# Kernel tuning notes

Measured on AMD Instinct MI355X. Metric: run time of the kernel, lower is better.

The kernel has to match this reference:

```python
import jax, jax.numpy as jnp
import numpy as np

N = 50000
F = 96
E = 800000
H = 2
DEPTH = 3
LEAKY_ALPHA = 0.2  # tf.nn.leaky_relu default


def setup_inputs() -> dict:
    key = jax.random.key(0)
    k1, k2, k3, k4, k5, k6 = jax.random.split(key, 6)
    node_f = jax.random.normal(k1, (N, F), dtype=jnp.float32)
    rows = jax.random.randint(k2, (E,), 0, N, dtype=jnp.int64)
    cols = jax.random.randint(k3, (E,), 0, N, dtype=jnp.int64)
    adj_idx = jnp.stack([rows, cols], axis=-1)[None]  # [1, E, 2]
    diag = jnp.arange(N, dtype=jnp.int64)
    adj_self_idx = jnp.stack([diag, diag], axis=-1)  # [N, 2] self loops
    adj_self_val = jax.random.uniform(k4, (N,), dtype=jnp.float32)
    attn_self_k = jax.random.normal(k5, (H, F), dtype=jnp.float32) * 0.05
    attn_neigh_k = jax.random.normal(k6, (H, F), dtype=jnp.float32) * 0.05
    return {"node_f": node_f, "adj_idx": adj_idx, "adj_self_idx": adj_self_idx,
            "adj_self_val": adj_self_val, "attn_self_k": attn_self_k,
            "attn_neigh_k": attn_neigh_k}


def _segment_softmax(scores, seg, n):
    # softmax over the nonzero entries of each row (tf.sparse_softmax semantics)
    m = jax.ops.segment_max(scores, seg, num_segments=n)
    ex = jnp.exp(scores - m[seg])
    denom = jax.ops.segment_sum(ex, seg, num_segments=n)
    return ex / denom[seg]


def reference(node_f, adj_idx, adj_self_idx, adj_self_val, attn_self_k, attn_neigh_k):
    rows = adj_idx[0, :, 0]
    cols = adj_idx[0, :, 1]
    s_rows = adj_self_idx[:, 0]
    s_cols = adj_self_idx[:, 1]
    # features = adj_self @ node_f (sparse matmul)
    features = jax.ops.segment_sum(adj_self_val[:, None] * node_f[s_cols],
                                   s_rows, num_segments=N)
    features = jax.nn.relu(features)
    outputs = [features]
    for _ in range(DEPTH):
        def head_fn(a_s, a_n, feats=features):
            e_self = feats @ a_s    # [N]
            e_neigh = feats @ a_n   # [N]
            scores = jax.nn.leaky_relu(e_self[rows] + e_neigh[cols], LEAKY_ALPHA)
            att = _segment_softmax(scores, rows, N)  # [E]
            return jax.ops.segment_sum(att[:, None] * feats[cols], rows,
                                       num_segments=N)  # [N, F]
        heads = jax.vmap(head_fn)(attn_self_k, attn_neigh_k)  # [H, N, F]
        features = jax.nn.relu(jnp.mean(heads, axis=0))
        outputs.append(features)
    return jnp.concatenate(outputs, axis=-1)  # [N, F*(DEPTH+1)]
```

## Files before the change

kernel.cpp:

```cpp
#include <hip/hip_runtime.h>
#include <math.h>

#define NN 50000
#define FF 96
#define EE 800000
#define OF 384
#define GB 3125
#define FBU 48
#define CAP 64
#define NB 196
#define BCAP 4608
#define CHUNK 4082
#define SHARD 12500

__device__ __forceinline__ float grp_sum(float v) {
    for (int m = 8; m >= 1; m >>= 1) v += __shfl_xor(v, m, 64);
    return v;
}
__device__ __forceinline__ float lrelu(float x) { return x > 0.f ? x : 0.2f * x; }
__device__ __forceinline__ float bf_lo(unsigned u) { return __uint_as_float(u << 16); }
__device__ __forceinline__ float bf_hi(unsigned u) { return __uint_as_float(u & 0xffff0000u); }
__device__ __forceinline__ unsigned pack_bf(float a, float b) {
    unsigned ua = __float_as_uint(a), ub = __float_as_uint(b);
    ua = ua + 0x7fffu + ((ua >> 16) & 1u);
    ub = ub + 0x7fffu + ((ub >> 16) & 1u);
    return (ua >> 16) | (ub & 0xffff0000u);
}

__device__ __forceinline__ float grp_dot8(const float* a,
                                          const float* __restrict__ kf, int lg) {
    float s = 0.f;
    if (lg < 12) {
        float4 w0 = ((const float4*)kf)[2 * lg];
        float4 w1 = ((const float4*)kf)[2 * lg + 1];
        s = a[0] * w0.x + a[1] * w0.y + a[2] * w0.z + a[3] * w0.w +
            a[4] * w1.x + a[5] * w1.y + a[6] * w1.z + a[7] * w1.w;
    }
    return grp_sum(s);
}

template<int BF>
__global__ __launch_bounds__(256) void l0_phase1(const float* __restrict__ node_f,
                                                 const int* __restrict__ sidx,
                                                 const float* __restrict__ sval,
                                                 float* __restrict__ out,
                                                 unsigned* __restrict__ fb,
                                                 const float* __restrict__ ks,
                                                 const float* __restrict__ kn,
                                                 float2* __restrict__ ass,
                                                 float2* __restrict__ ann,
                                                 const int2* __restrict__ idx2,
                                                 int* __restrict__ bfill,
                                                 unsigned* __restrict__ buckets) {
    __shared__ int cnt[NB], basearr[NB], ofs[NB];
    int tid = threadIdx.x;
    if (blockIdx.x < NB) {
        int p = blockIdx.x;
        int start = p * CHUNK, end = min(start + CHUNK, EE);
        if (tid < NB) { cnt[tid] = 0; ofs[tid] = 0; }
        __syncthreads();
        for (int e = start + tid; e < end; e += 256)
            atomicAdd(&cnt[idx2[e].x >> 8], 1);
        __syncthreads();
        if (tid < NB)
            basearr[tid] = cnt[tid] ? atomicAdd(&bfill[tid], cnt[tid]) : 0;
        __syncthreads();
        for (int e = start + tid; e < end; e += 256) {
            int2 q = idx2[e];
            int b = q.x >> 8;
            int slot = basearr[b] + atomicAdd(&ofs[b], 1);
            if (slot < BCAP)
                buckets[(size_t)b * BCAP + slot] =
                    ((unsigned)(q.x & 255) << 16) | (unsigned)q.y;
        }
        return;
    }
    int g = tid >> 4, lg = tid & 15;
    int n = (blockIdx.x - NB) * 16 + g;
    if (n >= NN) return;
    int sr = sidx[2 * n];
    int sc = sidx[2 * n + 1];
    float v = sval[n];
    float a[8] = {0.f, 0.f, 0.f, 0.f, 0.f, 0.f, 0.f, 0.f};
    if (lg < 12) {
        const float4* xr4 = (const float4*)(node_f + (size_t)sc * FF);
        float4 x0 = xr4[2 * lg], x1 = xr4[2 * lg + 1];
        a[0] = fmaxf(v * x0.x, 0.f); a[1] = fmaxf(v * x0.y, 0.f);
        a[2] = fmaxf(v * x0.z, 0.f); a[3] = fmaxf(v * x0.w, 0.f);
        a[4] = fmaxf(v * x1.x, 0.f); a[5] = fmaxf(v * x1.y, 0.f);
        a[6] = fmaxf(v * x1.z, 0.f); a[7] = fmaxf(v * x1.w, 0.f);
        float4* op4 = (float4*)(out + (size_t)sr * OF);
        op4[2 * lg]     = make_float4(a[0], a[1], a[2], a[3]);
        op4[2 * lg + 1] = make_float4(a[4], a[5], a[6], a[7]);
        if (BF) {
            uint4 p;
            p.x = pack_bf(a[0], a[1]); p.y = pack_bf(a[2], a[3]);
            p.z = pack_bf(a[4], a[5]); p.w = pack_bf(a[6], a[7]);
            ((uint4*)(fb + (size_t)sr * FBU))[lg] = p;
        }
    }
    float p0 = grp_dot8(a, ks, lg);
    float p1 = grp_dot8(a, ks + FF, lg);
    float p2 = grp_dot8(a, kn, lg);
    float p3 = grp_dot8(a, kn + FF, lg);
    if (lg == 0) {
        ass[sr] = make_float2(p0, p1);
        ann[sr] = make_float2(p2, p3);
    }
}

__global__ __launch_bounds__(256) void bucket2csr(const int* __restrict__ bfill,
                                                  const unsigned* __restrict__ buckets,
                                                  int* __restrict__ fill,
                                                  unsigned short* __restrict__ csr) {
    __shared__ unsigned short lcsr[64 * CAP];
    __shared__ int lcnt[64 * 4], loff[64 * 4];
    int tid = threadIdx.x, b = blockIdx.x >> 2, q = blockIdx.x & 3;
    lcnt[tid] = 0;
    __syncthreads();
    int cnt = min(bfill[b], BCAP);
    const unsigned* bp = buckets + (size_t)b * BCAP;
    for (int i = tid; i < cnt; i += 256) {
        unsigned u = bp[i];
        int lr = u >> 16;
        if ((lr >> 6) == q)
            atomicAdd(&lcnt[(lr & 63) * 4 + (int)((u & 0xffffu) / SHARD)], 1);
    }
    __syncthreads();
    if (tid < 64) {
        int c0 = lcnt[tid * 4], c1 = lcnt[tid * 4 + 1];
        int c2 = lcnt[tid * 4 + 2], c3 = lcnt[tid * 4 + 3];
        loff[tid * 4] = 0;
        loff[tid * 4 + 1] = c0;
        loff[tid * 4 + 2] = c0 + c1;
        loff[tid * 4 + 3] = c0 + c1 + c2;
        int r = b * 256 + q * 64 + tid;
        if (r < NN) fill[r] = min(c0 + c1 + c2 + c3, CAP);
        lcnt[tid * 4] = 0; lcnt[tid * 4 + 1] = 0;
        lcnt[tid * 4 + 2] = 0; lcnt[tid * 4 + 3] = 0;
    }
    __syncthreads();
    for (int i = tid; i < cnt; i += 256) {
        unsigned u = bp[i];
        int lr = u >> 16;
        if ((lr >> 6) != q) continue;
        int col = u & 0xffffu, cls = col / SHARD, lrl = lr & 63;
        int pos = loff[lrl * 4 + cls] + atomicAdd(&lcnt[lrl * 4 + cls], 1);
        if (pos < CAP) lcsr[lrl * CAP + pos] = (unsigned short)col;
    }
    __syncthreads();
    const uint4* src = (const uint4*)lcsr;
    uint4* dst = (uint4*)(csr + ((size_t)b * 256 + q * 64) * CAP);
    for (int i = tid; i < 64 * CAP / 8; i += 256) dst[i] = src[i];
}

template<int BF>
__device__ __forceinline__ void agg_chunk(float cj, int colj, int nj, int gbase,
                                          const float* __restrict__ feats,
                                          const unsigned* __restrict__ fb, int lg,
                                          float* a) {
#pragma unroll 8
    for (int k = 0; k < nj; ++k) {
        float cc = __shfl(cj, gbase + k, 64);
        int col  = __shfl(colj, gbase + k, 64);
        if (lg < 12) {
            if (BF) {
                uint4 q = ((const uint4*)(fb + (size_t)col * FBU))[lg];
                a[0] += cc * bf_lo(q.x); a[1] += cc * bf_hi(q.x);
                a[2] += cc * bf_lo(q.y); a[3] += cc * bf_hi(q.y);
                a[4] += cc * bf_lo(q.z); a[5] += cc * bf_hi(q.z);
                a[6] += cc * bf_lo(q.w); a[7] += cc * bf_hi(q.w);
            } else {
                const float4* vp = (const float4*)(feats + (size_t)col * OF);
                float4 v0 = vp[2 * lg], v1 = vp[2 * lg + 1];
                a[0] += cc * v0.x; a[1] += cc * v0.y;
                a[2] += cc * v0.z; a[3] += cc * v0.w;
                a[4] += cc * v1.x; a[5] += cc * v1.y;
                a[6] += cc * v1.z; a[7] += cc * v1.w;
            }
        }
    }
}

template<int BF>
__global__ __launch_bounds__(256) void gat_layer(float* __restrict__ out, int l,
                                                 const int* __restrict__ fill,
                                                 const unsigned short* __restrict__ csr,
                                                 const float2* __restrict__ ass,
                                                 const float2* __restrict__ ann,
                                                 const unsigned* __restrict__ fb_in,
                                                 unsigned* __restrict__ fb_out,
                                                 const float* __restrict__ ks,
                                                 const float* __restrict__ kn,
                                                 float2* __restrict__ ass_out,
                                                 float2* __restrict__ ann_out,
                                                 int write_dots) {
    int tid = threadIdx.x;
    int g = tid >> 4, lg = tid & 15;
    int gbase = (g & 3) * 16;
    int r = blockIdx.x * 16 + g;
    if (r >= NN) return;
    int deg = fill[r];
    const unsigned short* crow = csr + (size_t)r * CAP;
    const float* feats = out + l * FF;
    float2 as_r = ass[r];

    float d0 = 0.f, d1 = 0.f;
    int   c0col = 0, c1col = 0;
    float e00 = 0.f, e01 = 0.f, e10 = 0.f, e11 = 0.f;
    if (lg < deg) {
        int c = crow[lg];
        float2 an = ann[c];
        c0col = c;
        e00 = __expf(lrelu(as_r.x + an.x));
        e01 = __expf(lrelu(as_r.y + an.y));
        d0 += e00; d1 += e01;
    }
    if (deg > 16) {
        int j = 16 + lg;
        if (j < deg) {
            int c = crow[j];
            float2 an = ann[c];
            c1col = c;
            e10 = __expf(lrelu(as_r.x + an.x));
            e11 = __expf(lrelu(as_r.y + an.y));
            d0 += e10; d1 += e11;
        }
        for (int j0 = 32; j0 < deg; j0 += 16) {
            int jj = j0 + lg;
            if (jj < deg) {
                float2 an = ann[crow[jj]];
                d0 += __expf(lrelu(as_r.x + an.x));
                d1 += __expf(lrelu(as_r.y + an.y));
            }
        }
    }
    d0 = grp_sum(d0);
    d1 = grp_sum(d1);
    float inv0 = d0 > 0.f ? 0.5f / d0 : 0.f;
    float inv1 = d1 > 0.f ? 0.5f / d1 : 0.f;

    float a[8] = {0.f, 0.f, 0.f, 0.f, 0.f, 0.f, 0.f, 0.f};
    agg_chunk<BF>(e00 * inv0 + e01 * inv1, c0col, min(deg, 16), gbase,
                  feats, fb_in, lg, a);
    if (deg > 16) {
        agg_chunk<BF>(e10 * inv0 + e11 * inv1, c1col, min(deg - 16, 16), gbase,
                      feats, fb_in, lg, a);
        for (int j0 = 32; j0 < deg; j0 += 16) {
            float cjr = 0.f; int colr = 0;
            int jj = j0 + lg;
            if (jj < deg) {
                int c = crow[jj];
                float2 an = ann[c];
                cjr = __expf(lrelu(as_r.x + an.x)) * inv0 +
                      __expf(lrelu(as_r.y + an.y)) * inv1;
                colr = c;
            }
            agg_chunk<BF>(cjr, colr, min(deg - j0, 16), gbase, feats, fb_in, lg, a);
        }
    }

#pragma unroll
    for (int i = 0; i < 8; ++i) a[i] = fmaxf(a[i], 0.f);
    if (lg < 12) {
        float4* op4 = (float4*)(out + (size_t)r * OF + (l + 1) * FF);
        op4[2 * lg]     = make_float4(a[0], a[1], a[2], a[3]);
        op4[2 * lg + 1] = make_float4(a[4], a[5], a[6], a[7]);
        if (BF && fb_out) {
            uint4 p;
            p.x = pack_bf(a[0], a[1]); p.y = pack_bf(a[2], a[3]);
            p.z = pack_bf(a[4], a[5]); p.w = pack_bf(a[6], a[7]);
            ((uint4*)(fb_out + (size_t)r * FBU))[lg] = p;
        }
    }

    if (write_dots) {
        float p0 = grp_dot8(a, ks, lg);
        float p1 = grp_dot8(a, ks + FF, lg);
        float p2 = grp_dot8(a, kn, lg);
        float p3 = grp_dot8(a, kn + FF, lg);
        if (lg == 0) {
            ass_out[r] = make_float2(p0, p1);
            ann_out[r] = make_float2(p2, p3);
        }
    }
}

extern "C" void kernel_launch(void* const* d_in, const int* in_sizes, int n_in,
                              void* d_out, int out_size, void* d_ws, size_t ws_size,
                              hipStream_t stream) {
    const float* node_f  = (const float*)d_in[0];
    const int*   adj_idx = (const int*)d_in[1];
    const int*   sidx    = (const int*)d_in[2];
    const float* sval    = (const float*)d_in[3];
    const float* k_self  = (const float*)d_in[4];
    const float* k_neigh = (const float*)d_in[5];
    float* out = (float*)d_out;

    char* w = (char*)d_ws;
    auto alloc = [&](size_t bytes) {
        char* p = w;
        w += (bytes + 255) & ~(size_t)255;
        return p;
    };
    int*            fill    = (int*)alloc((size_t)NN * 4);
    unsigned short* csr     = (unsigned short*)alloc((size_t)NB * 256 * CAP * 2);
    int*            bfill   = (int*)alloc((size_t)NB * 4);
    unsigned*       buckets = (unsigned*)alloc((size_t)NB * BCAP * 4);
    float2*         ass_a   = (float2*)alloc((size_t)NN * 8);
    float2*         ann_a   = (float2*)alloc((size_t)NN * 8);
    float2*         ass_b   = (float2*)alloc((size_t)NN * 8);
    float2*         ann_b   = (float2*)alloc((size_t)NN * 8);
    unsigned*       fb_a    = (unsigned*)alloc((size_t)NN * FBU * 4);
    unsigned*       fb_b    = (unsigned*)alloc((size_t)NN * FBU * 4);
    bool bf = (size_t)(w - (char*)d_ws) <= ws_size;

    hipMemsetAsync(bfill, 0, (size_t)NB * 4, stream);

    if (bf) {
        l0_phase1<1><<<NB + GB, 256, 0, stream>>>(node_f, sidx, sval, out, fb_a,
                                                  k_self, k_neigh, ass_a, ann_a,
                                                  (const int2*)adj_idx, bfill, buckets);
        bucket2csr<<<NB * 4, 256, 0, stream>>>(bfill, buckets, fill, csr);
        gat_layer<1><<<GB, 256, 0, stream>>>(out, 0, fill, csr, ass_a, ann_a,
                                             fb_a, fb_b, k_self, k_neigh,
                                             ass_b, ann_b, 1);
        gat_layer<1><<<GB, 256, 0, stream>>>(out, 1, fill, csr, ass_b, ann_b,
                                             fb_b, fb_a, k_self, k_neigh,
                                             ass_a, ann_a, 1);
        gat_layer<1><<<GB, 256, 0, stream>>>(out, 2, fill, csr, ass_a, ann_a,
                                             fb_a, nullptr, k_self, k_neigh,
                                             ass_b, ann_b, 0);
    } else {
        l0_phase1<0><<<NB + GB, 256, 0, stream>>>(node_f, sidx, sval, out, nullptr,
                                                  k_self, k_neigh, ass_a, ann_a,
                                                  (const int2*)adj_idx, bfill, buckets);
        bucket2csr<<<NB * 4, 256, 0, stream>>>(bfill, buckets, fill, csr);
        gat_layer<0><<<GB, 256, 0, stream>>>(out, 0, fill, csr, ass_a, ann_a,
                                             nullptr, nullptr, k_self, k_neigh,
                                             ass_b, ann_b, 1);
        gat_layer<0><<<GB, 256, 0, stream>>>(out, 1, fill, csr, ass_b, ann_b,
                                             nullptr, nullptr, k_self, k_neigh,
                                             ass_a, ann_a, 1);
        gat_layer<0><<<GB, 256, 0, stream>>>(out, 2, fill, csr, ass_a, ann_a,
                                             nullptr, nullptr, k_self, k_neigh,
                                             ass_b, ann_b, 0);
    }
}
```

Measured before the change: 231.0 us.

## Sort rows by degree within 64-row groups to balance GAT aggregation work

bucket2csr now ranks each 64-row group by degree and writes the CSR rows and fill counts in sorted order, along with an rmap from sorted slot to original row. gat_layer processes rows in this permuted order and looks up the real row through rmap. The aim is for rows sharing a wavefront (four 16-lane groups) to have similar degrees, which reduces divergence and idle lanes in the neighbour loops. The cost is an extra indirection per row, scattered output writes, and a small O(64) rank computation per block.

```diff
diff --git a/kernel.cpp b/kernel.cpp
--- a/kernel.cpp
+++ b/kernel.cpp
@@ -9,6 +9,7 @@
 #define FBU 48
 #define CAP 64
 #define NB 196
+#define NR 50176
 #define BCAP 4608
 #define CHUNK 4082
 #define SHARD 12500
@@ -112,10 +113,13 @@
 __global__ __launch_bounds__(256) void bucket2csr(const int* __restrict__ bfill,
                                                   const unsigned* __restrict__ buckets,
                                                   int* __restrict__ fill,
-                                                  unsigned short* __restrict__ csr) {
+                                                  unsigned short* __restrict__ csr,
+                                                  int* __restrict__ rmap) {
     __shared__ unsigned short lcsr[64 * CAP];
     __shared__ int lcnt[64 * 4], loff[64 * 4];
+    __shared__ int sdeg[64], srank[64];
     int tid = threadIdx.x, b = blockIdx.x >> 2, q = blockIdx.x & 3;
+    int base = b * 256 + q * 64;
     lcnt[tid] = 0;
     __syncthreads();
     int cnt = min(bfill[b], BCAP);
@@ -127,6 +131,7 @@
             atomicAdd(&lcnt[(lr & 63) * 4 + (int)((u & 0xffffu) / SHARD)], 1);
     }
     __syncthreads();
+    int mydeg = 0;
     if (tid < 64) {
         int c0 = lcnt[tid * 4], c1 = lcnt[tid * 4 + 1];
         int c2 = lcnt[tid * 4 + 2], c3 = lcnt[tid * 4 + 3];
@@ -134,10 +139,21 @@
         loff[tid * 4 + 1] = c0;
         loff[tid * 4 + 2] = c0 + c1;
         loff[tid * 4 + 3] = c0 + c1 + c2;
-        int r = b * 256 + q * 64 + tid;
-        if (r < NN) fill[r] = min(c0 + c1 + c2 + c3, CAP);
+        mydeg = min(c0 + c1 + c2 + c3, CAP);
+        sdeg[tid] = (base + tid < NN) ? mydeg : 0x7fffffff;
         lcnt[tid * 4] = 0; lcnt[tid * 4 + 1] = 0;
         lcnt[tid * 4 + 2] = 0; lcnt[tid * 4 + 3] = 0;
+    }
+    __syncthreads();
+    if (tid < 64) {
+        int key = sdeg[tid], rank = 0;
+        for (int i = 0; i < 64; ++i) {
+            int ki = sdeg[i];
+            rank += (ki < key) || (ki == key && i < tid);
+        }
+        srank[tid] = rank;
+        fill[base + rank] = mydeg;
+        rmap[base + rank] = base + tid;
     }
     __syncthreads();
     for (int i = tid; i < cnt; i += 256) {
@@ -150,8 +166,11 @@
     }
     __syncthreads();
     const uint4* src = (const uint4*)lcsr;
-    uint4* dst = (uint4*)(csr + ((size_t)b * 256 + q * 64) * CAP);
-    for (int i = tid; i < 64 * CAP / 8; i += 256) dst[i] = src[i];
+    uint4* dst = (uint4*)csr;
+    for (int i = tid; i < 64 * (CAP / 8); i += 256) {
+        int row = i >> 3, chunk = i & 7;
+        dst[(size_t)(base + srank[row]) * (CAP / 8) + chunk] = src[i];
+    }
 }
 
 template<int BF>
@@ -186,6 +205,7 @@
 __global__ __launch_bounds__(256) void gat_layer(float* __restrict__ out, int l,
                                                  const int* __restrict__ fill,
                                                  const unsigned short* __restrict__ csr,
+                                                 const int* __restrict__ rmap,
                                                  const float2* __restrict__ ass,
                                                  const float2* __restrict__ ann,
                                                  const unsigned* __restrict__ fb_in,
@@ -198,10 +218,11 @@
     int tid = threadIdx.x;
     int g = tid >> 4, lg = tid & 15;
     int gbase = (g & 3) * 16;
-    int r = blockIdx.x * 16 + g;
-    if (r >= NN) return;
-    int deg = fill[r];
-    const unsigned short* crow = csr + (size_t)r * CAP;
+    int idx = blockIdx.x * 16 + g;
+    if (idx >= NN) return;
+    int r = rmap[idx];
+    int deg = fill[idx];
+    const unsigned short* crow = csr + (size_t)idx * CAP;
     const float* feats = out + l * FF;
     float2 as_r = ass[r];
 
@@ -303,8 +324,9 @@
         w += (bytes + 255) & ~(size_t)255;
         return p;
     };
-    int*            fill    = (int*)alloc((size_t)NN * 4);
-    unsigned short* csr     = (unsigned short*)alloc((size_t)NB * 256 * CAP * 2);
+    int*            fill    = (int*)alloc((size_t)NR * 4);
+    int*            rmap    = (int*)alloc((size_t)NR * 4);
+    unsigned short* csr     = (unsigned short*)alloc((size_t)NR * CAP * 2);
     int*            bfill   = (int*)alloc((size_t)NB * 4);
     unsigned*       buckets = (unsigned*)alloc((size_t)NB * BCAP * 4);
     float2*         ass_a   = (float2*)alloc((size_t)NN * 8);
@@ -321,28 +343,28 @@
         l0_phase1<1><<<NB + GB, 256, 0, stream>>>(node_f, sidx, sval, out, fb_a,
                                                   k_self, k_neigh, ass_a, ann_a,
                                                   (const int2*)adj_idx, bfill, buckets);
-        bucket2csr<<<NB * 4, 256, 0, stream>>>(bfill, buckets, fill, csr);
-        gat_layer<1><<<GB, 256, 0, stream>>>(out, 0, fill, csr, ass_a, ann_a,
+        bucket2csr<<<NB * 4, 256, 0, stream>>>(bfill, buckets, fill, csr, rmap);
+        gat_layer<1><<<GB, 256, 0, stream>>>(out, 0, fill, csr, rmap, ass_a, ann_a,
                                              fb_a, fb_b, k_self, k_neigh,
                                              ass_b, ann_b, 1);
-        gat_layer<1><<<GB, 256, 0, stream>>>(out, 1, fill, csr, ass_b, ann_b,
+        gat_layer<1><<<GB, 256, 0, stream>>>(out, 1, fill, csr, rmap, ass_b, ann_b,
                                              fb_b, fb_a, k_self, k_neigh,
                                              ass_a, ann_a, 1);
-        gat_layer<1><<<GB, 256, 0, stream>>>(out, 2, fill, csr, ass_a, ann_a,
+        gat_layer<1><<<GB, 256, 0, stream>>>(out, 2, fill, csr, rmap, ass_a, ann_a,
                                              fb_a, nullptr, k_self, k_neigh,
                                              ass_b, ann_b, 0);
     } else {
         l0_phase1<0><<<NB + GB, 256, 0, stream>>>(node_f, sidx, sval, out, nullptr,
                                                   k_self, k_neigh, ass_a, ann_a,
                                                   (const int2*)adj_idx, bfill, buckets);
-        bucket2csr<<<NB * 4, 256, 0, stream>>>(bfill, buckets, fill, csr);
-        gat_layer<0><<<GB, 256, 0, stream>>>(out, 0, fill, csr, ass_a, ann_a,
+        bucket2csr<<<NB * 4, 256, 0, stream>>>(bfill, buckets, fill, csr, rmap);
+        gat_layer<0><<<GB, 256, 0, stream>>>(out, 0, fill, csr, rmap, ass_a, ann_a,
                                              nullptr, nullptr, k_self, k_neigh,
                                              ass_b, ann_b, 1);
-        gat_layer<0><<<GB, 256, 0, stream>>>(out, 1, fill, csr, ass_b, ann_b,
+        gat_layer<0><<<GB, 256, 0, stream>>>(out, 1, fill, csr, rmap, ass_b, ann_b,
                                              nullptr, nullptr, k_self, k_neigh,
                                              ass_a, ann_a, 1);
-        gat_layer<0><<<GB, 256, 0, stream>>>(out, 2, fill, csr, ass_a, ann_a,
+        gat_layer<0><<<GB, 256, 0, stream>>>(out, 2, fill, csr, rmap, ass_a, ann_a,
                                              nullptr, nullptr, k_self, k_neigh,
                                              ass_b, ann_b, 0);
     }
```

Result: no change. 233.3 us (+1.0%).

## Fuse softmax denominator into single-pass aggregation with per-head accumulators

Applied to the files above, without the earlier changes.

Replaces the two-pass scheme (compute exp scores in parallel across lanes, reduce the denominator, then broadcast weights via shuffles) with a single loop over neighbors. Every lane loads each column index and score and computes both heads' exponentials redundantly, accumulating unnormalized sums in two 8-wide accumulators. Normalization happens once at the end. This removes the shuffles, the group reductions and the second read of the CSR and attention arrays, at the cost of redundant exp work per lane and twice the accumulator registers.

```diff
diff --git a/kernel.cpp b/kernel.cpp
--- a/kernel.cpp
+++ b/kernel.cpp
@@ -155,34 +155,6 @@
 }
 
 template<int BF>
-__device__ __forceinline__ void agg_chunk(float cj, int colj, int nj, int gbase,
-                                          const float* __restrict__ feats,
-                                          const unsigned* __restrict__ fb, int lg,
-                                          float* a) {
-#pragma unroll 8
-    for (int k = 0; k < nj; ++k) {
-        float cc = __shfl(cj, gbase + k, 64);
-        int col  = __shfl(colj, gbase + k, 64);
-        if (lg < 12) {
-            if (BF) {
-                uint4 q = ((const uint4*)(fb + (size_t)col * FBU))[lg];
-                a[0] += cc * bf_lo(q.x); a[1] += cc * bf_hi(q.x);
-                a[2] += cc * bf_lo(q.y); a[3] += cc * bf_hi(q.y);
-                a[4] += cc * bf_lo(q.z); a[5] += cc * bf_hi(q.z);
-                a[6] += cc * bf_lo(q.w); a[7] += cc * bf_hi(q.w);
-            } else {
-                const float4* vp = (const float4*)(feats + (size_t)col * OF);
-                float4 v0 = vp[2 * lg], v1 = vp[2 * lg + 1];
-                a[0] += cc * v0.x; a[1] += cc * v0.y;
-                a[2] += cc * v0.z; a[3] += cc * v0.w;
-                a[4] += cc * v1.x; a[5] += cc * v1.y;
-                a[6] += cc * v1.z; a[7] += cc * v1.w;
-            }
-        }
-    }
-}
-
-template<int BF>
 __global__ __launch_bounds__(256) void gat_layer(float* __restrict__ out, int l,
                                                  const int* __restrict__ fill,
                                                  const unsigned short* __restrict__ csr,
@@ -197,7 +169,6 @@
                                                  int write_dots) {
     int tid = threadIdx.x;
     int g = tid >> 4, lg = tid & 15;
-    int gbase = (g & 3) * 16;
     int r = blockIdx.x * 16 + g;
     if (r >= NN) return;
     int deg = fill[r];
@@ -205,63 +176,53 @@
     const float* feats = out + l * FF;
     float2 as_r = ass[r];
 
+    float A0[8] = {0.f, 0.f, 0.f, 0.f, 0.f, 0.f, 0.f, 0.f};
+    float A1[8] = {0.f, 0.f, 0.f, 0.f, 0.f, 0.f, 0.f, 0.f};
     float d0 = 0.f, d1 = 0.f;
-    int   c0col = 0, c1col = 0;
-    float e00 = 0.f, e01 = 0.f, e10 = 0.f, e11 = 0.f;
-    if (lg < deg) {
-        int c = crow[lg];
-        float2 an = ann[c];
-        c0col = c;
-        e00 = __expf(lrelu(as_r.x + an.x));
-        e01 = __expf(lrelu(as_r.y + an.y));
-        d0 += e00; d1 += e01;
-    }
-    if (deg > 16) {
-        int j = 16 + lg;
-        if (j < deg) {
-            int c = crow[j];
-            float2 an = ann[c];
-            c1col = c;
-            e10 = __expf(lrelu(as_r.x + an.x));
-            e11 = __expf(lrelu(as_r.y + an.y));
-            d0 += e10; d1 += e11;
-        }
-        for (int j0 = 32; j0 < deg; j0 += 16) {
-            int jj = j0 + lg;
-            if (jj < deg) {
-                float2 an = ann[crow[jj]];
-                d0 += __expf(lrelu(as_r.x + an.x));
-                d1 += __expf(lrelu(as_r.y + an.y));
+#pragma unroll 8
+    for (int k = 0; k < deg; ++k) {
+        int col = crow[k];
+        float2 an = ann[col];
+        float e0 = __expf(lrelu(as_r.x + an.x));
+        float e1 = __expf(lrelu(as_r.y + an.y));
+        d0 += e0; d1 += e1;
+        if (lg < 12) {
+            if (BF) {
+                uint4 qv = ((const uint4*)(fb_in + (size_t)col * FBU))[lg];
+                float f0 = bf_lo(qv.x), f1 = bf_hi(qv.x);
+                float f2 = bf_lo(qv.y), f3 = bf_hi(qv.y);
+                float f4 = bf_lo(qv.z), f5 = bf_hi(qv.z);
+                float f6 = bf_lo(qv.w), f7 = bf_hi(qv.w);
+                A0[0] += e0 * f0; A1[0] += e1 * f0;
+                A0[1] += e0 * f1; A1[1] += e1 * f1;
+                A0[2] += e0 * f2; A1[2] += e1 * f2;
+                A0[3] += e0 * f3; A1[3] += e1 * f3;
+                A0[4] += e0 * f4; A1[4] += e1 * f4;
+                A0[5] += e0 * f5; A1[5] += e1 * f5;
+                A0[6] += e0 * f6; A1[6] += e1 * f6;
+                A0[7] += e0 * f7; A1[7] += e1 * f7;
+            } else {
+                const float4* vp = (const float4*)(feats + (size_t)col * OF);
+                float4 v0 = vp[2 * lg], v1 = vp[2 * lg + 1];
+                A0[0] += e0 * v0.x; A1[0] += e1 * v0.x;
+                A0[1] += e0 * v0.y; A1[1] += e1 * v0.y;
+                A0[2] += e0 * v0.z; A1[2] += e1 * v0.z;
+                A0[3] += e0 * v0.w; A1[3] += e1 * v0.w;
+                A0[4] += e0 * v1.x; A1[4] += e1 * v1.x;
+                A0[5] += e0 * v1.y; A1[5] += e1 * v1.y;
+                A0[6] += e0 * v1.z; A1[6] += e1 * v1.z;
+                A0[7] += e0 * v1.w; A1[7] += e1 * v1.w;
             }
         }
     }
-    d0 = grp_sum(d0);
-    d1 = grp_sum(d1);
     float inv0 = d0 > 0.f ? 0.5f / d0 : 0.f;
     float inv1 = d1 > 0.f ? 0.5f / d1 : 0.f;
 
-    float a[8] = {0.f, 0.f, 0.f, 0.f, 0.f, 0.f, 0.f, 0.f};
-    agg_chunk<BF>(e00 * inv0 + e01 * inv1, c0col, min(deg, 16), gbase,
-                  feats, fb_in, lg, a);
-    if (deg > 16) {
-        agg_chunk<BF>(e10 * inv0 + e11 * inv1, c1col, min(deg - 16, 16), gbase,
-                      feats, fb_in, lg, a);
-        for (int j0 = 32; j0 < deg; j0 += 16) {
-            float cjr = 0.f; int colr = 0;
-            int jj = j0 + lg;
-            if (jj < deg) {
-                int c = crow[jj];
-                float2 an = ann[c];
-                cjr = __expf(lrelu(as_r.x + an.x)) * inv0 +
-                      __expf(lrelu(as_r.y + an.y)) * inv1;
-                colr = c;
-            }
-            agg_chunk<BF>(cjr, colr, min(deg - j0, 16), gbase, feats, fb_in, lg, a);
-        }
-    }
-
+    float a[8];
 #pragma unroll
-    for (int i = 0; i < 8; ++i) a[i] = fmaxf(a[i], 0.f);
+    for (int i = 0; i < 8; ++i)
+        a[i] = fmaxf(A0[i] * inv0 + A1[i] * inv1, 0.f);
+
     if (lg < 12) {
         float4* op4 = (float4*)(out + (size_t)r * OF + (l + 1) * FF);
         op4[2 * lg]     = make_float4(a[0], a[1], a[2], a[3]);
```

Measured after the change: 294.4 us. +27.4%, slower.
